# Kernel optimization log

Hardware: AMD Instinct MI355X
Metric: run time of the kernel (lower is better)

## Reference

```python
import jax, jax.numpy as jnp
import numpy as np

N, E, Q = 50000, 500000, 100000
IN_DIM, HID, EDGE_DIM, NUM_CLASSES = 128, 128, 16, 2


def _glorot(key, shape):
    fan_in, fan_out = shape
    lim = (6.0 / (fan_in + fan_out)) ** 0.5
    return jax.random.uniform(key, shape, jnp.float32, -lim, lim)


def setup_inputs() -> dict:
    key = jax.random.key(0)
    ks = jax.random.split(key, 12)
    return {
        "node_feature": jax.random.normal(ks[0], (N, IN_DIM), jnp.float32),
        "edge_index": jax.random.randint(ks[1], (2, E), 0, N, jnp.int64),
        "edge_feature": jax.random.normal(ks[2], (E, EDGE_DIM), jnp.float32),
        "edge_label_index": jax.random.randint(ks[3], (2, Q), 0, N, jnp.int64),
        # conv1 params
        "c1_pre_W": _glorot(ks[4], (IN_DIM, IN_DIM)),
        "c1_pre_b": jnp.zeros((IN_DIM,), jnp.float32),
        "c1_msg_W": _glorot(ks[5], (2 * IN_DIM + EDGE_DIM, HID)),
        "c1_msg_b": jnp.zeros((HID,), jnp.float32),
        # conv2 params
        "c2_pre_W": _glorot(ks[6], (HID, HID)),
        "c2_pre_b": jnp.zeros((HID,), jnp.float32),
        "c2_msg_W": _glorot(ks[7], (2 * HID + EDGE_DIM, HID)),
        "c2_msg_b": jnp.zeros((HID,), jnp.float32),
        # link-prediction head
        "lp_W": _glorot(ks[8], (2 * HID, NUM_CLASSES)),
        "lp_b": jnp.zeros((NUM_CLASSES,), jnp.float32),
    }


def _mlp_message_conv(x, edge_index, edge_feature, pre_W, pre_b, msg_W, msg_b):
    # pre_conv: Linear + ReLU
    h = jax.nn.relu(x @ pre_W + pre_b)
    src, dst = edge_index[0], edge_index[1]
    # PyG default flow source_to_target: x_i = target, x_j = source
    x_i = h[dst]  # [E, d]
    x_j = h[src]  # [E, d]
    msg = jnp.concatenate([x_i, x_j, edge_feature], axis=1) @ msg_W + msg_b  # [E, out]
    # aggr='add' onto target nodes
    return jax.ops.segment_sum(msg, dst, num_segments=x.shape[0])


def reference(node_feature, edge_index, edge_feature, edge_label_index,
              c1_pre_W, c1_pre_b, c1_msg_W, c1_msg_b,
              c2_pre_W, c2_pre_b, c2_msg_W, c2_msg_b,
              lp_W, lp_b):
    # eval mode: dropout is identity
    x = jax.nn.relu(_mlp_message_conv(node_feature, edge_index, edge_feature,
                                      c1_pre_W, c1_pre_b, c1_msg_W, c1_msg_b))
    x = _mlp_message_conv(x, edge_index, edge_feature,
                          c2_pre_W, c2_pre_b, c2_msg_W, c2_msg_b)
    nodes_first = x[edge_label_index[0]]   # [Q, hid]
    nodes_second = x[edge_label_index[1]]  # [Q, hid]
    pred = jnp.concatenate([nodes_first, nodes_second], axis=-1) @ lp_W + lp_b
    return pred
```

## Files before the change

kernel.cpp:

```cpp
#include <hip/hip_runtime.h>
#include <cstdint>
#include <cstddef>


typedef __attribute__((ext_vector_type(8))) short short8;
typedef __attribute__((ext_vector_type(4))) float float4v;

__device__ __forceinline__ ushort f2b(float f) {
    uint u = __float_as_uint(f);
    u = u + 0x7fff + ((u >> 16) & 1);
    return (ushort)(u >> 16);
}
__device__ __forceinline__ float b2f(ushort h) {
    return __uint_as_float(((uint)h) << 16);
}
__device__ __forceinline__ uint pack2(float a, float b) {
    return (uint)f2b(a) | ((uint)f2b(b) << 16);
}

#define F_MSG     1
#define F_RELU    2
#define F_DEGBIAS 4
#define F_OUTB    8
#define F_IN32    16
#define F_HEAD    32

#define XS_STRIDE 72

__launch_bounds__(256, 2)
__global__ void gemm_mfma(const ushort* __restrict__ A, const ushort* __restrict__ B,
                          const ushort* __restrict__ EF, const float* __restrict__ A32,
                          const float* __restrict__ DEG, const ushort* __restrict__ Wt,
                          const float* __restrict__ bias, ushort* __restrict__ outB,
                          const float* __restrict__ lpW, float* __restrict__ z,
                          int M, int Kp, int flags)
{
    __shared__ ushort xs[128 * XS_STRIDE];
    __shared__ ushort ws[128 * XS_STRIDE];
    const int tid  = threadIdx.x;
    const int lane = tid & 63;
    const int wave = tid >> 6;
    const int row0 = blockIdx.x << 7;

    float4v acc[2][8];
#pragma unroll
    for (int m = 0; m < 2; ++m)
#pragma unroll
        for (int t = 0; t < 8; ++t) acc[m][t] = (float4v){0.f, 0.f, 0.f, 0.f};

    const int arow0 = (wave << 5) + (lane & 15);
    const int koff  = (lane >> 4) << 3;
    const int bcol  = lane & 15;

    for (int kt = 0; kt < Kp; kt += 64) {
        __syncthreads();
        for (int idx = tid; idx < 128 * 8; idx += 256) {
            const int n = idx >> 3;
            const int g = idx & 7;
            const uint4 v = *(const uint4*)&Wt[(size_t)n * Kp + kt + (g << 3)];
            *(uint4*)&ws[n * XS_STRIDE + (g << 3)] = v;
        }
        if (flags & F_MSG) {
            for (int idx = tid; idx < 128 * 8; idx += 256) {
                const int r  = idx >> 3;
                const int g  = idx & 7;
                const int gr = row0 + r;
                const int kk = kt + (g << 3);
                uint4 v = make_uint4(0, 0, 0, 0);
                if (gr < M) {
                    if (kk < 128) {
                        uint4 a = *(const uint4*)&A[((size_t)gr << 7) + kk];
                        const float d = DEG[gr];
                        uint* p = (uint*)&a;
#pragma unroll
                        for (int q = 0; q < 4; ++q)
                            p[q] = pack2(b2f((ushort)(p[q] & 0xffff)) * d,
                                         b2f((ushort)(p[q] >> 16)) * d);
                        v = a;
                    } else if (kk < 256) {
                        v = *(const uint4*)&B[((size_t)gr << 7) + kk - 128];
                    } else if (kk < 272) {
                        v = *(const uint4*)&EF[((size_t)gr << 4) + kk - 256];
                    }
                }
                *(uint4*)&xs[r * XS_STRIDE + (g << 3)] = v;
            }
        } else if (flags & F_IN32) {
            for (int idx = tid; idx < 128 * 8; idx += 256) {
                const int r  = idx >> 3;
                const int g  = idx & 7;
                const int gr = row0 + r;
                uint4 v = make_uint4(0, 0, 0, 0);
                if (gr < M) {
                    const float4 f0 = *(const float4*)&A32[((size_t)gr << 7) + kt + (g << 3)];
                    const float4 f1 = *(const float4*)&A32[((size_t)gr << 7) + kt + (g << 3) + 4];
                    v.x = pack2(f0.x, f0.y); v.y = pack2(f0.z, f0.w);
                    v.z = pack2(f1.x, f1.y); v.w = pack2(f1.z, f1.w);
                }
                *(uint4*)&xs[r * XS_STRIDE + (g << 3)] = v;
            }
        } else {
            for (int idx = tid; idx < 128 * 8; idx += 256) {
                const int r  = idx >> 3;
                const int g  = idx & 7;
                const int gr = row0 + r;
                uint4 v = make_uint4(0, 0, 0, 0);
                if (gr < M) v = *(const uint4*)&A[((size_t)gr << 7) + kt + (g << 3)];
                *(uint4*)&xs[r * XS_STRIDE + (g << 3)] = v;
            }
        }
        __syncthreads();
#pragma unroll
        for (int s = 0; s < 64; s += 32) {
            const short8 a0 = *(const short8*)&xs[arow0 * XS_STRIDE + s + koff];
            const short8 a1 = *(const short8*)&xs[(arow0 + 16) * XS_STRIDE + s + koff];
#pragma unroll
            for (int t = 0; t < 8; ++t) {
                const short8 bf = *(const short8*)&ws[((t << 4) + bcol) * XS_STRIDE + s + koff];
                acc[0][t] = __builtin_amdgcn_mfma_f32_16x16x32_bf16(a0, bf, acc[0][t], 0, 0, 0);
                acc[1][t] = __builtin_amdgcn_mfma_f32_16x16x32_bf16(a1, bf, acc[1][t], 0, 0, 0);
            }
        }
    }

    float bcv[8];
#pragma unroll
    for (int t = 0; t < 8; ++t) bcv[t] = bias[(t << 4) + bcol];

    if (flags & F_HEAD) {
        const float2* lw = (const float2*)lpW;
        float2 wa[8], wb[8];
#pragma unroll
        for (int t = 0; t < 8; ++t) {
            const int col = (t << 4) + bcol;
            wa[t] = lw[col];
            wb[t] = lw[128 + col];
        }
#pragma unroll
        for (int m = 0; m < 2; ++m) {
            const int rbase = row0 + (wave << 5) + (m << 4) + ((lane >> 4) << 2);
#pragma unroll
            for (int r = 0; r < 4; ++r) {
                const int row = rbase + r;
                const float d = (row < M) ? DEG[row] : 0.f;
                float za0 = 0.f, za1 = 0.f, zb0 = 0.f, zb1 = 0.f;
#pragma unroll
                for (int t = 0; t < 8; ++t) {
                    const float v = acc[m][t][r] + d * bcv[t];
                    za0 += v * wa[t].x; za1 += v * wa[t].y;
                    zb0 += v * wb[t].x; zb1 += v * wb[t].y;
                }
#pragma unroll
                for (int mk = 8; mk > 0; mk >>= 1) {
                    za0 += __shfl_xor(za0, mk);
                    za1 += __shfl_xor(za1, mk);
                    zb0 += __shfl_xor(zb0, mk);
                    zb1 += __shfl_xor(zb1, mk);
                }
                if (bcol == 0 && row < M)
                    *(float4*)&z[(size_t)row * 4] = make_float4(za0, za1, zb0, zb1);
            }
        }
    } else {
#pragma unroll
        for (int m = 0; m < 2; ++m) {
            const int rbase = row0 + (wave << 5) + (m << 4) + ((lane >> 4) << 2);
#pragma unroll
            for (int t = 0; t < 8; ++t) {
                const int col = (t << 4) + bcol;
#pragma unroll
                for (int r = 0; r < 4; ++r) {
                    const int row = rbase + r;
                    if (row >= M) continue;
                    float v = acc[m][t][r];
                    v += (flags & F_DEGBIAS) ? DEG[row] * bcv[t] : bcv[t];
                    if (flags & F_RELU) v = fmaxf(v, 0.f);
                    outB[((size_t)row << 7) + col] = f2b(v);
                }
            }
        }
    }
}

__launch_bounds__(256)
__global__ void prep(const float* __restrict__ c1pW, const float* __restrict__ c2pW,
                     const float* __restrict__ c1mW, const float* __restrict__ c2mW,
                     ushort* __restrict__ wtp1, ushort* __restrict__ wtp2,
                     ushort* __restrict__ wtm1, ushort* __restrict__ wtm2,
                     int* __restrict__ counts, int N)
{
    const int gtid = blockIdx.x * 256 + threadIdx.x;
    const int gstr = gridDim.x * 256;
    for (int i = gtid; i < N; i += gstr) counts[i] = 0;
    for (int idx = gtid; idx < 128 * 128; idx += gstr) {
        const int n = idx >> 7, k = idx & 127;
        wtp1[idx] = f2b(c1pW[(size_t)k * 128 + n]);
        wtp2[idx] = f2b(c2pW[(size_t)k * 128 + n]);
    }
    for (int idx = gtid; idx < 128 * 320; idx += gstr) {
        const int n = idx / 320, k = idx - n * 320;
        wtm1[idx] = (k < 272) ? f2b(c1mW[(size_t)k * 128 + n]) : (ushort)0;
        wtm2[idx] = (k < 272) ? f2b(c2mW[(size_t)k * 128 + n]) : (ushort)0;
    }
}

__launch_bounds__(256)
__global__ void hist_kernel(const int* __restrict__ ei, int* __restrict__ counts, int E)
{
    const int e = blockIdx.x * 256 + threadIdx.x;
    if (e < E) atomicAdd(&counts[ei[E + e]], 1);
}

__launch_bounds__(256)
__global__ void scan_phase1(const int* __restrict__ counts, int* __restrict__ rowstart,
                            int* __restrict__ blocksums, int N)
{
    __shared__ int sdata[256];
    const int t = threadIdx.x;
    const int i = blockIdx.x * 256 + t;
    const int v = (i < N) ? counts[i] : 0;
    sdata[t] = v;
    __syncthreads();
    for (int off = 1; off < 256; off <<= 1) {
        const int add = (t >= off) ? sdata[t - off] : 0;
        __syncthreads();
        sdata[t] += add;
        __syncthreads();
    }
    if (i < N) rowstart[i] = sdata[t] - v;
    if (t == 255) blocksums[blockIdx.x] = sdata[255];
}

__launch_bounds__(256)
__global__ void scan_phase23(const int* __restrict__ counts, const int* __restrict__ bs,
                             int* __restrict__ rowstart, int* __restrict__ cursor,
                             float* __restrict__ degf, int N, int E)
{
    __shared__ int sdata[256];
    const int t = threadIdx.x;
    const int vb = blockIdx.x;
    int part = 0;
    for (int j = t; j < vb; j += 256) part += bs[j];
    sdata[t] = part;
    __syncthreads();
    for (int s = 128; s > 0; s >>= 1) {
        if (t < s) sdata[t] += sdata[t + s];
        __syncthreads();
    }
    const int off = sdata[0];
    const int i = vb * 256 + t;
    if (i < N) {
        const int rs = rowstart[i] + off;
        rowstart[i] = rs;
        cursor[i]   = rs;
        degf[i]     = (float)counts[i];
    }
    if (vb == 0 && t == 0) rowstart[N] = E;
}

__launch_bounds__(256)
__global__ void build_elist(const int* __restrict__ ei, int* __restrict__ cursor,
                            int2* __restrict__ elist, int E)
{
    const int e = blockIdx.x * 256 + threadIdx.x;
    if (e >= E) return;
    const int d = ei[E + e];
    const int pos = atomicAdd(&cursor[d], 1);
    elist[pos] = make_int2(ei[e], e);
}

__launch_bounds__(256)
__global__ void gather(const int2* __restrict__ elist, const int* __restrict__ rowstart,
                       const ushort* __restrict__ h, ushort* __restrict__ agg,
                       const float* __restrict__ ef, ushort* __restrict__ aggef,
                       int N, int doEf)
{
    const int tid = threadIdx.x;
    if (doEf) {
        const int nvb = (N + 15) / 16;
        const int lane16 = tid & 15;
        for (int vb = blockIdx.x; vb < nvb; vb += gridDim.x) {
            const int node = vb * 16 + (tid >> 4);
            if (node >= N) continue;
            const int beg = rowstart[node];
            const int end = rowstart[node + 1];
            float acc = 0.f;
            for (int k = beg; k < end; ++k)
                acc += ef[((size_t)elist[k].y << 4) + lane16];
            aggef[((size_t)node << 4) + lane16] = f2b(acc);
        }
    }
    {
        const int nvb = (N + 7) / 8;
        const int grp = tid >> 5;
        const int l   = tid & 31;
        for (int vb = blockIdx.x; vb < nvb; vb += gridDim.x) {
            const int node = vb * 8 + grp;
            if (node >= N) continue;
            const int beg = rowstart[node];
            const int end = rowstart[node + 1];
            float a0 = 0.f, a1 = 0.f, a2 = 0.f, a3 = 0.f;
            int k = beg;
            for (; k + 7 < end; k += 8) {
                uint2 v[8];
#pragma unroll
                for (int j = 0; j < 8; ++j) {
                    const int s = elist[k + j].x;
                    v[j] = *(const uint2*)&h[((size_t)s << 7) + (l << 2)];
                }
#pragma unroll
                for (int j = 0; j < 8; ++j) {
                    a0 += b2f((ushort)(v[j].x & 0xffff));
                    a1 += b2f((ushort)(v[j].x >> 16));
                    a2 += b2f((ushort)(v[j].y & 0xffff));
                    a3 += b2f((ushort)(v[j].y >> 16));
                }
            }
            for (; k < end; ++k) {
                const uint2 v = *(const uint2*)&h[((size_t)elist[k].x << 7) + (l << 2)];
                a0 += b2f((ushort)(v.x & 0xffff));
                a1 += b2f((ushort)(v.x >> 16));
                a2 += b2f((ushort)(v.y & 0xffff));
                a3 += b2f((ushort)(v.y >> 16));
            }
            uint2 o;
            o.x = pack2(a0, a1);
            o.y = pack2(a2, a3);
            *(uint2*)&agg[((size_t)node << 7) + (l << 2)] = o;
        }
    }
}

__launch_bounds__(256)
__global__ void head_kernel(const float4* __restrict__ z, const int* __restrict__ eli,
                            const float* __restrict__ lpb, float* __restrict__ out, int Q)
{
    const int q = blockIdx.x * 256 + threadIdx.x;
    if (q >= Q) return;
    const int a = eli[q];
    const int b = eli[Q + q];
    const float4 za = z[a];
    const float4 zb = z[b];
    float2 o = make_float2(za.x + zb.z + lpb[0], za.y + zb.w + lpb[1]);
    *(float2*)&out[(size_t)q * 2] = o;
}

extern "C" void kernel_launch(void* const* d_in, const int* in_sizes, int n_in,
                              void* d_out, int out_size, void* d_ws, size_t ws_size,
                              hipStream_t stream)
{
    const float* nf   = (const float*)d_in[0];
    const int*   ei   = (const int*)d_in[1];
    const float* ef   = (const float*)d_in[2];
    const int*   eli  = (const int*)d_in[3];
    const float* c1pW = (const float*)d_in[4];
    const float* c1pb = (const float*)d_in[5];
    const float* c1mW = (const float*)d_in[6];
    const float* c1mb = (const float*)d_in[7];
    const float* c2pW = (const float*)d_in[8];
    const float* c2pb = (const float*)d_in[9];
    const float* c2mW = (const float*)d_in[10];
    const float* c2mb = (const float*)d_in[11];
    const float* lpW  = (const float*)d_in[12];
    const float* lpb  = (const float*)d_in[13];
    float* out = (float*)d_out;

    const int N = in_sizes[0] / 128;
    const int E = in_sizes[1] / 2;
    const int Q = in_sizes[3] / 2;

    float* DEG = (float*)d_ws;
    float* z   = DEG + N;
    int* counts    = (int*)(z + (size_t)N * 4);
    int* rowstart  = counts + N;
    int* cursor    = rowstart + N + 1;
    int* blocksums = cursor + N;
    uintptr_t ep8 = (uintptr_t)(blocksums + 1024);
    ep8 = (ep8 + 7) & ~(uintptr_t)7;
    int2* elist = (int2*)ep8;
    uintptr_t up = (uintptr_t)(elist + E);
    up = (up + 15) & ~(uintptr_t)15;
    ushort* h_bf   = (ushort*)up;
    ushort* agg_bf = h_bf   + (size_t)N * 128;
    ushort* x1_bf  = agg_bf + (size_t)N * 128;
    ushort* ef_bf  = x1_bf  + (size_t)N * 128;
    ushort* wtp1   = ef_bf  + (size_t)N * 16;
    ushort* wtm1   = wtp1 + 128 * 128;
    ushort* wtp2   = wtm1 + 128 * 320;
    ushort* wtm2   = wtp2 + 128 * 128;

    const int gemmGrid = (N + 127) / 128;
    const int eGrid    = (E + 255) / 256;
    const int nGrid    = (N + 255) / 256;
    const int gGrid    = (N + 7) / 8;
    const int headGrid = (Q + 255) / 256;

    prep<<<nGrid, 256, 0, stream>>>(c1pW, c2pW, c1mW, c2mW, wtp1, wtp2, wtm1, wtm2,
                                    counts, N);
    hist_kernel<<<eGrid, 256, 0, stream>>>(ei, counts, E);
    scan_phase1<<<nGrid, 256, 0, stream>>>(counts, rowstart, blocksums, N);
    scan_phase23<<<nGrid, 256, 0, stream>>>(counts, blocksums, rowstart, cursor, DEG, N, E);
    build_elist<<<eGrid, 256, 0, stream>>>(ei, cursor, elist, E);

    gemm_mfma<<<gemmGrid, 256, 0, stream>>>(nullptr, nullptr, nullptr, nf, DEG, wtp1,
                                            c1pb, h_bf, nullptr, nullptr, N, 128,
                                            F_RELU | F_OUTB | F_IN32);
    gather<<<gGrid, 256, 0, stream>>>(elist, rowstart, h_bf, agg_bf, ef, ef_bf, N, 1);
    gemm_mfma<<<gemmGrid, 256, 0, stream>>>(h_bf, agg_bf, ef_bf, nullptr, DEG, wtm1,
                                            c1mb, x1_bf, nullptr, nullptr, N, 320,
                                            F_MSG | F_RELU | F_DEGBIAS | F_OUTB);

    gemm_mfma<<<gemmGrid, 256, 0, stream>>>(x1_bf, nullptr, nullptr, nullptr, DEG, wtp2,
                                            c2pb, h_bf, nullptr, nullptr, N, 128,
                                            F_RELU | F_OUTB);
    gather<<<gGrid, 256, 0, stream>>>(elist, rowstart, h_bf, agg_bf, nullptr, nullptr, N, 0);
    gemm_mfma<<<gemmGrid, 256, 0, stream>>>(h_bf, agg_bf, ef_bf, nullptr, DEG, wtm2,
                                            c2mb, nullptr, lpW, z, N, 320,
                                            F_MSG | F_DEGBIAS | F_HEAD);

    head_kernel<<<headGrid, 256, 0, stream>>>((const float4*)z, eli, lpb, out, Q);
}
```

Before: 327.8 us.

## Partition gather feature columns by XCD and schedule chunks with atomic tickets

The neighbour-aggregation gather now splits the 128-wide bf16 feature rows into four 32-column slices. Each block reads its hardware XCC id and starts on the matching slice, so each XCD's L2 mostly holds one quarter of the node-feature matrix instead of the whole table. Work is handed out in 64-node chunks through per-slice atomic tickets, which are zeroed in prep, on a fixed 2048-block grid. Each thread now loads 16-byte vectors covering 8 features. The costs are two barriers plus one atomic per chunk, and a dependency on an undocumented hwreg read for the XCC id.

```diff
diff --git a/kernel.cpp b/kernel.cpp
--- a/kernel.cpp
+++ b/kernel.cpp
@@ -16,6 +16,11 @@
 }
 __device__ __forceinline__ uint pack2(float a, float b) {
     return (uint)f2b(a) | ((uint)f2b(b) << 16);
+}
+__device__ __forceinline__ int xcc_id() {
+    int x;
+    asm volatile("s_getreg_b32 %0, hwreg(20, 0, 4)" : "=s"(x));
+    return x;
 }
 
 #define F_MSG     1
@@ -187,10 +192,11 @@
                      const float* __restrict__ c1mW, const float* __restrict__ c2mW,
                      ushort* __restrict__ wtp1, ushort* __restrict__ wtp2,
                      ushort* __restrict__ wtm1, ushort* __restrict__ wtm2,
-                     int* __restrict__ counts, int N)
+                     int* __restrict__ counts, int* __restrict__ tickets, int N)
 {
     const int gtid = blockIdx.x * 256 + threadIdx.x;
     const int gstr = gridDim.x * 256;
+    if (gtid < 8) tickets[gtid] = 0;
     for (int i = gtid; i < N; i += gstr) counts[i] = 0;
     for (int idx = gtid; idx < 128 * 128; idx += gstr) {
         const int n = idx >> 7, k = idx & 127;
@@ -273,7 +279,7 @@
 __global__ void gather(const int2* __restrict__ elist, const int* __restrict__ rowstart,
                        const ushort* __restrict__ h, ushort* __restrict__ agg,
                        const float* __restrict__ ef, ushort* __restrict__ aggef,
-                       int N, int doEf)
+                       int* __restrict__ tickets, int tbase, int N, int doEf)
 {
     const int tid = threadIdx.x;
     if (doEf) {
@@ -290,43 +296,66 @@
             aggef[((size_t)node << 4) + lane16] = f2b(acc);
         }
     }
-    {
-        const int nvb = (N + 7) / 8;
-        const int grp = tid >> 5;
-        const int l   = tid & 31;
-        for (int vb = blockIdx.x; vb < nvb; vb += gridDim.x) {
-            const int node = vb * 8 + grp;
+
+    __shared__ int s_chunk;
+    const int nchunks = (N + 63) / 64;
+    const int pref = xcc_id() & 3;
+    const int grp = tid >> 2;
+    const int l   = tid & 3;
+    const int co  = l << 3;
+
+    for (int si = 0; si < 4; ++si) {
+        const int slice = (pref + si) & 3;
+        const int sbase = slice << 5;
+        while (true) {
+            __syncthreads();
+            if (tid == 0) s_chunk = atomicAdd(&tickets[tbase + slice], 1);
+            __syncthreads();
+            const int c = s_chunk;
+            if (c >= nchunks) break;
+            const int node = c * 64 + grp;
             if (node >= N) continue;
             const int beg = rowstart[node];
             const int end = rowstart[node + 1];
-            float a0 = 0.f, a1 = 0.f, a2 = 0.f, a3 = 0.f;
+            float a0 = 0.f, a1 = 0.f, a2 = 0.f, a3 = 0.f,
+                  a4 = 0.f, a5 = 0.f, a6 = 0.f, a7 = 0.f;
             int k = beg;
-            for (; k + 7 < end; k += 8) {
-                uint2 v[8];
-#pragma unroll
-                for (int j = 0; j < 8; ++j) {
+            for (; k + 3 < end; k += 4) {
+                uint4 v[4];
+#pragma unroll
+                for (int j = 0; j < 4; ++j) {
                     const int s = elist[k + j].x;
-                    v[j] = *(const uint2*)&h[((size_t)s << 7) + (l << 2)];
-                }
-#pragma unroll
-                for (int j = 0; j < 8; ++j) {
+                    v[j] = *(const uint4*)&h[((size_t)s << 7) + sbase + co];
+                }
+#pragma unroll
+                for (int j = 0; j < 4; ++j) {
                     a0 += b2f((ushort)(v[j].x & 0xffff));
                     a1 += b2f((ushort)(v[j].x >> 16));
                     a2 += b2f((ushort)(v[j].y & 0xffff));
                     a3 += b2f((ushort)(v[j].y >> 16));
+                    a4 += b2f((ushort)(v[j].z & 0xffff));
+                    a5 += b2f((ushort)(v[j].z >> 16));
+                    a6 += b2f((ushort)(v[j].w & 0xffff));
+                    a7 += b2f((ushort)(v[j].w >> 16));
                 }
             }
             for (; k < end; ++k) {
-                const uint2 v = *(const uint2*)&h[((size_t)elist[k].x << 7) + (l << 2)];
+                const uint4 v = *(const uint4*)&h[((size_t)elist[k].x << 7) + sbase + co];
                 a0 += b2f((ushort)(v.x & 0xffff));
                 a1 += b2f((ushort)(v.x >> 16));
                 a2 += b2f((ushort)(v.y & 0xffff));
                 a3 += b2f((ushort)(v.y >> 16));
-            }
-            uint2 o;
+                a4 += b2f((ushort)(v.z & 0xffff));
+                a5 += b2f((ushort)(v.z >> 16));
+                a6 += b2f((ushort)(v.w & 0xffff));
+                a7 += b2f((ushort)(v.w >> 16));
+            }
+            uint4 o;
             o.x = pack2(a0, a1);
             o.y = pack2(a2, a3);
-            *(uint2*)&agg[((size_t)node << 7) + (l << 2)] = o;
+            o.z = pack2(a4, a5);
+            o.w = pack2(a6, a7);
+            *(uint4*)&agg[((size_t)node << 7) + sbase + co] = o;
         }
     }
 }
@@ -375,6 +404,7 @@
     int* rowstart  = counts + N;
     int* cursor    = rowstart + N + 1;
     int* blocksums = cursor + N;
+    int* tickets   = blocksums + 512;
     uintptr_t ep8 = (uintptr_t)(blocksums + 1024);
     ep8 = (ep8 + 7) & ~(uintptr_t)7;
     int2* elist = (int2*)ep8;
@@ -392,11 +422,11 @@
     const int gemmGrid = (N + 127) / 128;
     const int eGrid    = (E + 255) / 256;
     const int nGrid    = (N + 255) / 256;
-    const int gGrid    = (N + 7) / 8;
+    const int gGrid    = 2048;
     const int headGrid = (Q + 255) / 256;
 
     prep<<<nGrid, 256, 0, stream>>>(c1pW, c2pW, c1mW, c2mW, wtp1, wtp2, wtm1, wtm2,
-                                    counts, N);
+                                    counts, tickets, N);
     hist_kernel<<<eGrid, 256, 0, stream>>>(ei, counts, E);
     scan_phase1<<<nGrid, 256, 0, stream>>>(counts, rowstart, blocksums, N);
     scan_phase23<<<nGrid, 256, 0, stream>>>(counts, blocksums, rowstart, cursor, DEG, N, E);
@@ -405,7 +435,8 @@
     gemm_mfma<<<gemmGrid, 256, 0, stream>>>(nullptr, nullptr, nullptr, nf, DEG, wtp1,
                                             c1pb, h_bf, nullptr, nullptr, N, 128,
                                             F_RELU | F_OUTB | F_IN32);
-    gather<<<gGrid, 256, 0, stream>>>(elist, rowstart, h_bf, agg_bf, ef, ef_bf, N, 1);
+    gather<<<gGrid, 256, 0, stream>>>(elist, rowstart, h_bf, agg_bf, ef, ef_bf,
+                                      tickets, 0, N, 1);
     gemm_mfma<<<gemmGrid, 256, 0, stream>>>(h_bf, agg_bf, ef_bf, nullptr, DEG, wtm1,
                                             c1mb, x1_bf, nullptr, nullptr, N, 320,
                                             F_MSG | F_RELU | F_DEGBIAS | F_OUTB);
@@ -413,7 +444,8 @@
     gemm_mfma<<<gemmGrid, 256, 0, stream>>>(x1_bf, nullptr, nullptr, nullptr, DEG, wtp2,
                                             c2pb, h_bf, nullptr, nullptr, N, 128,
                                             F_RELU | F_OUTB);
-    gather<<<gGrid, 256, 0, stream>>>(elist, rowstart, h_bf, agg_bf, nullptr, nullptr, N, 0);
+    gather<<<gGrid, 256, 0, stream>>>(elist, rowstart, h_bf, agg_bf, nullptr, nullptr,
+                                      tickets, 4, N, 0);
     gemm_mfma<<<gemmGrid, 256, 0, stream>>>(h_bf, agg_bf, ef_bf, nullptr, DEG, wtm2,
                                             c2mb, nullptr, lpW, z, N, 320,
                                             F_MSG | F_DEGBIAS | F_HEAD);
```

Result: slower. 561.0 us (+71.1%).
